# Kernel optimization log

Measured on AMD Instinct MI355X. Metric: run time of the kernel, lower is better.

## Reference

```python
import jax, jax.numpy as jnp
import numpy as np


def _pairwise_sqdist(x, y):
    # x: [B, N, D], y: [B, M, D] -> P: [B, N, M] squared euclidean distances
    xx = jnp.sum(x * x, axis=-1)              # [B, N]
    yy = jnp.sum(y * y, axis=-1)              # [B, M]
    zz = jnp.einsum('bnd,bmd->bnm', x, y)     # [B, N, M]
    return xx[:, :, None] + yy[:, None, :] - 2.0 * zz


def setup_inputs() -> dict:
    key = jax.random.key(0)
    k1, k2 = jax.random.split(key)
    B, N, D = 8, 8192, 3
    preds = jax.random.normal(k1, (B, N, D), dtype=jnp.float32)
    gts = jax.random.normal(k2, (B, N, D), dtype=jnp.float32)
    return {"preds": preds, "gts": gts}


def reference(preds, gts):
    # P = batch_pairwise_dist(gts, preds): P[b, i, j] = ||gts[b,i] - preds[b,j]||^2
    P = _pairwise_sqdist(gts, preds)          # [B, N_gts, N_preds]
    loss_1 = jnp.sum(jnp.min(P, axis=1))      # min over gts points
    loss_2 = jnp.sum(jnp.min(P, axis=2))      # min over pred points
    return loss_1 + loss_2
```

## Files before the change

### kernel.cpp

```cpp
#include <hip/hip_runtime.h>

typedef _Float16 f16;
typedef f16 half8 __attribute__((ext_vector_type(8)));
typedef float f32x16 __attribute__((ext_vector_type(16)));

#define BB 8
#define NN 8192
#define SETPTS (BB * NN)
#define NPTS (2 * SETPTS)
#define TQ NPTS

__device__ __forceinline__ void gload_lds16(const void* g, void* l) {
  __builtin_amdgcn_global_load_lds(
      (const __attribute__((address_space(1))) void*)g,
      (__attribute__((address_space(3))) void*)l, 16, 0, 0);
}

__global__ __launch_bounds__(256) void chamfer_prep(
    const float* __restrict__ preds, const float* __restrict__ gts,
    float* __restrict__ yy, half8* __restrict__ Aq, half8* __restrict__ Bq) {
  int idx = blockIdx.x * 256 + threadIdx.x;
  int s = idx >> 16;
  int off = idx & (SETPTS - 1);
  const float* src = s ? gts : preds;
  float x0 = src[off * 3 + 0], x1 = src[off * 3 + 1], x2 = src[off * 3 + 2];

  f16 h0 = (f16)x0; f16 l0 = (f16)(x0 - (float)h0);
  f16 h1 = (f16)x1; f16 l1 = (f16)(x1 - (float)h1);
  f16 h2 = (f16)x2; f16 l2 = (f16)(x2 - (float)h2);

  float Y0 = -2.f * x0, Y1 = -2.f * x1, Y2 = -2.f * x2;
  f16 H0 = (f16)Y0; f16 L0 = (f16)(Y0 - (float)H0);
  f16 H1 = (f16)Y1; f16 L1 = (f16)(Y1 - (float)H1);
  f16 H2 = (f16)Y2; f16 L2 = (f16)(Y2 - (float)H2);

  float yv = x0 * x0 + x1 * x1 + x2 * x2;
  f16 yh = (f16)yv; f16 yl = (f16)(yv - (float)yh);

  f16 one = (f16)1.f, zz = (f16)0.f;
  half8 A0 = {h0, l0, h0, l0, h1, l1, h1, l1};
  half8 A1 = {h2, l2, h2, l2, one, one, zz, zz};
  half8 B0 = {H0, H0, L0, L0, H1, H1, L1, L1};
  half8 B1 = {H2, H2, L2, L2, yh, yl, zz, zz};

  Aq[idx * 2 + 0] = A0; Aq[idx * 2 + 1] = A1;
  Bq[idx * 2 + 0] = B0; Bq[idx * 2 + 1] = B1;
  yy[idx] = yv;
}

template <int R>
__global__ __launch_bounds__(256, 4) void chamfer_mfma(
    const half8* __restrict__ Aq, const half8* __restrict__ Bq,
    float* __restrict__ partial) {
  constexpr int NSTEP = NN / R / 32;
  __shared__ __align__(16) char lds[NSTEP * 1024];

  int bi = blockIdx.x;
  int xcd = bi & 7;
  int idx = bi >> 3;
  int panel = xcd * 2 + (idx & 1);
  int dir = panel >> 3;
  int b = panel & 7;
  int sub = idx >> 1;
  int qb = sub & 31;
  int r = sub >> 5;

  int tid = threadIdx.x;
  int w = tid >> 6;
  int l = tid & 63;
  int l31 = l & 31;
  int lh = l >> 5;

  const half8* Qp =
      Aq + ((size_t)(dir * BB + b) * NN + qb * 256 + w * 64) * 2;
  half8 q0 = Qp[l31 * 2 + lh];
  half8 q1 = Qp[(32 + l31) * 2 + lh];

  const char* gpanel = (const char*)(Bq + ((size_t)((1 - dir) * BB + b) * NN +
                                           r * (NN / R)) * 2);
  int perm = ((l & 31) * 2 + (l >> 5)) * 16;

  {
    constexpr int TPW = NSTEP / 4;
    const char* csrc = gpanel + (size_t)(w * TPW) * 1024 + perm;
    char* cdst = &lds[w * TPW * 1024];
#pragma unroll
    for (int i = 0; i < TPW; ++i)
      gload_lds16(csrc + i * 1024, cdst + i * 1024);
  }

  f32x16 zero;
#pragma unroll
  for (int i = 0; i < 16; ++i) zero[i] = 0.f;
  float run0 = 3.4e38f, run1 = 3.4e38f;

  __syncthreads();

  const half8* lb = (const half8*)&lds[0];
#pragma unroll 4
  for (int st = 0; st < NSTEP; ++st) {
    half8 bt = lb[st * 64 + l];
    f32x16 oa = __builtin_amdgcn_mfma_f32_32x32x16_f16(bt, q0, zero, 0, 0, 0);
    f32x16 ob = __builtin_amdgcn_mfma_f32_32x32x16_f16(bt, q1, zero, 0, 0, 0);
    {
      float t0 = fminf(fminf(oa[0], oa[1]), oa[2]);
      float t1 = fminf(fminf(oa[3], oa[4]), oa[5]);
      float t2 = fminf(fminf(oa[6], oa[7]), oa[8]);
      float t3 = fminf(fminf(oa[9], oa[10]), oa[11]);
      float t4 = fminf(fminf(oa[12], oa[13]), oa[14]);
      float u0 = fminf(fminf(t0, t1), t2);
      float u1 = fminf(fminf(t3, t4), oa[15]);
      run0 = fminf(fminf(run0, u0), u1);
    }
    {
      float t0 = fminf(fminf(ob[0], ob[1]), ob[2]);
      float t1 = fminf(fminf(ob[3], ob[4]), ob[5]);
      float t2 = fminf(fminf(ob[6], ob[7]), ob[8]);
      float t3 = fminf(fminf(ob[9], ob[10]), ob[11]);
      float t4 = fminf(fminf(ob[12], ob[13]), ob[14]);
      float u0 = fminf(fminf(t0, t1), t2);
      float u1 = fminf(fminf(t3, t4), ob[15]);
      run1 = fminf(fminf(run1, u0), u1);
    }
  }

  float v0 = fminf(run0, __shfl_xor(run0, 32));
  float v1 = fminf(run1, __shfl_xor(run1, 32));

  size_t qflat = (size_t)(dir * BB + b) * NN + qb * 256 + w * 64;
  float* pr = partial + (size_t)r * TQ + qflat;
  if (lh == 0) {
    pr[l31] = v0;
    pr[32 + l31] = v1;
  }
}

template <int R>
__global__ __launch_bounds__(256) void chamfer_combine(
    const float* __restrict__ partial, const float* __restrict__ yy,
    float* __restrict__ bsums) {
  int q = blockIdx.x * 256 + threadIdx.x;
  float m = partial[q];
#pragma unroll
  for (int rr = 1; rr < R; ++rr) m = fminf(m, partial[(size_t)rr * TQ + q]);
  m += yy[q];
  __shared__ float s[256];
  s[threadIdx.x] = m;
  __syncthreads();
  for (int o = 128; o > 0; o >>= 1) {
    if (threadIdx.x < o) s[threadIdx.x] += s[threadIdx.x + o];
    __syncthreads();
  }
  if (threadIdx.x == 0) bsums[blockIdx.x] = s[0];
}

__global__ __launch_bounds__(256) void chamfer_final(
    const float* __restrict__ bsums, float* __restrict__ out, int n) {
  float v = 0.f;
  for (int i = threadIdx.x; i < n; i += 256) v += bsums[i];
  __shared__ float s[256];
  s[threadIdx.x] = v;
  __syncthreads();
  for (int o = 128; o > 0; o >>= 1) {
    if (threadIdx.x < o) s[threadIdx.x] += s[threadIdx.x + o];
    __syncthreads();
  }
  if (threadIdx.x == 0) out[0] = s[0];
}

extern "C" void kernel_launch(void* const* d_in, const int* in_sizes, int n_in,
                              void* d_out, int out_size, void* d_ws,
                              size_t ws_size, hipStream_t stream) {
  const float* preds = (const float*)d_in[0];
  const float* gts = (const float*)d_in[1];
  float* out = (float*)d_out;

  size_t fixed = (size_t)1024 * 4 + (size_t)NPTS * 4 + (size_t)NPTS * 64;
  int R = (ws_size >= (size_t)16 * TQ * 4 + fixed) ? 16 : 8;

  float* partial = (float*)d_ws;
  float* bsums = partial + (size_t)R * TQ;
  float* yy = bsums + 1024;
  half8* Aq = (half8*)(yy + NPTS);
  half8* Bq = Aq + (size_t)NPTS * 2;

  chamfer_prep<<<NPTS / 256, 256, 0, stream>>>(preds, gts, yy, Aq, Bq);
  if (R == 16) {
    chamfer_mfma<16><<<2 * BB * 32 * 16, 256, 0, stream>>>(Aq, Bq, partial);
    chamfer_combine<16><<<TQ / 256, 256, 0, stream>>>(partial, yy, bsums);
  } else {
    chamfer_mfma<8><<<2 * BB * 32 * 8, 256, 0, stream>>>(Aq, Bq, partial);
    chamfer_combine<8><<<TQ / 256, 256, 0, stream>>>(partial, yy, bsums);
  }
  chamfer_final<<<1, 256, 0, stream>>>(bsums, out, TQ / 256);
}
```

Before: 48.65 us.

## Stream reference tiles from global into registers instead of staging in LDS

The MFMA kernel no longer stages its reference panel into LDS with global_load_lds and a barrier. Each lane now loads its B fragment directly from global memory, with a two-step register prefetch across an unroll-by-two loop. The split factor R is fixed at 4, giving fewer blocks with longer loops and a smaller partial buffer for the combine pass. This removes LDS use and the block barrier, at the cost of relying on cache hits for the repeated global fragment loads and on fewer blocks to hide latency.

```diff
diff --git a/kernel.cpp b/kernel.cpp
--- a/kernel.cpp
+++ b/kernel.cpp
@@ -9,12 +9,6 @@
 #define SETPTS (BB * NN)
 #define NPTS (2 * SETPTS)
 #define TQ NPTS
-
-__device__ __forceinline__ void gload_lds16(const void* g, void* l) {
-  __builtin_amdgcn_global_load_lds(
-      (const __attribute__((address_space(1))) void*)g,
-      (__attribute__((address_space(3))) void*)l, 16, 0, 0);
-}
 
 __global__ __launch_bounds__(256) void chamfer_prep(
     const float* __restrict__ preds, const float* __restrict__ gts,
@@ -53,7 +47,6 @@
     const half8* __restrict__ Aq, const half8* __restrict__ Bq,
     float* __restrict__ partial) {
   constexpr int NSTEP = NN / R / 32;
-  __shared__ __align__(16) char lds[NSTEP * 1024];
 
   int bi = blockIdx.x;
   int xcd = bi & 7;
@@ -76,53 +69,49 @@
   half8 q0 = Qp[l31 * 2 + lh];
   half8 q1 = Qp[(32 + l31) * 2 + lh];
 
-  const char* gpanel = (const char*)(Bq + ((size_t)((1 - dir) * BB + b) * NN +
-                                           r * (NN / R)) * 2);
-  int perm = ((l & 31) * 2 + (l >> 5)) * 16;
-
-  {
-    constexpr int TPW = NSTEP / 4;
-    const char* csrc = gpanel + (size_t)(w * TPW) * 1024 + perm;
-    char* cdst = &lds[w * TPW * 1024];
-#pragma unroll
-    for (int i = 0; i < TPW; ++i)
-      gload_lds16(csrc + i * 1024, cdst + i * 1024);
-  }
+  const half8* Bl = Bq +
+                    ((size_t)((1 - dir) * BB + b) * NN + r * (NN / R)) * 2 +
+                    l31 * 2 + lh;
 
   f32x16 zero;
 #pragma unroll
   for (int i = 0; i < 16; ++i) zero[i] = 0.f;
   float run0 = 3.4e38f, run1 = 3.4e38f;
 
-  __syncthreads();
+#define MINTREE(o, run)                                   \
+  {                                                       \
+    float t0_ = fminf(fminf(o[0], o[1]), o[2]);           \
+    float t1_ = fminf(fminf(o[3], o[4]), o[5]);           \
+    float t2_ = fminf(fminf(o[6], o[7]), o[8]);           \
+    float t3_ = fminf(fminf(o[9], o[10]), o[11]);         \
+    float t4_ = fminf(fminf(o[12], o[13]), o[14]);        \
+    float u0_ = fminf(fminf(t0_, t1_), t2_);              \
+    float u1_ = fminf(fminf(t3_, t4_), o[15]);            \
+    run = fminf(fminf(run, u0_), u1_);                    \
+  }
 
-  const half8* lb = (const half8*)&lds[0];
-#pragma unroll 4
-  for (int st = 0; st < NSTEP; ++st) {
-    half8 bt = lb[st * 64 + l];
-    f32x16 oa = __builtin_amdgcn_mfma_f32_32x32x16_f16(bt, q0, zero, 0, 0, 0);
-    f32x16 ob = __builtin_amdgcn_mfma_f32_32x32x16_f16(bt, q1, zero, 0, 0, 0);
+  half8 t0 = Bl[0];
+  half8 t1 = Bl[64];
+#pragma unroll 1
+  for (int s = 0; s < NSTEP; s += 2) {
+    half8 t2 = Bl[(size_t)(((s + 2) & (NSTEP - 1)) * 64)];
     {
-      float t0 = fminf(fminf(oa[0], oa[1]), oa[2]);
-      float t1 = fminf(fminf(oa[3], oa[4]), oa[5]);
-      float t2 = fminf(fminf(oa[6], oa[7]), oa[8]);
-      float t3 = fminf(fminf(oa[9], oa[10]), oa[11]);
-      float t4 = fminf(fminf(oa[12], oa[13]), oa[14]);
-      float u0 = fminf(fminf(t0, t1), t2);
-      float u1 = fminf(fminf(t3, t4), oa[15]);
-      run0 = fminf(fminf(run0, u0), u1);
+      f32x16 oa = __builtin_amdgcn_mfma_f32_32x32x16_f16(t0, q0, zero, 0, 0, 0);
+      f32x16 ob = __builtin_amdgcn_mfma_f32_32x32x16_f16(t0, q1, zero, 0, 0, 0);
+      MINTREE(oa, run0)
+      MINTREE(ob, run1)
     }
+    half8 t3 = Bl[(size_t)(((s + 3) & (NSTEP - 1)) * 64)];
     {
-      float t0 = fminf(fminf(ob[0], ob[1]), ob[2]);
-      float t1 = fminf(fminf(ob[3], ob[4]), ob[5]);
-      float t2 = fminf(fminf(ob[6], ob[7]), ob[8]);
-      float t3 = fminf(fminf(ob[9], ob[10]), ob[11]);
-      float t4 = fminf(fminf(ob[12], ob[13]), ob[14]);
-      float u0 = fminf(fminf(t0, t1), t2);
-      float u1 = fminf(fminf(t3, t4), ob[15]);
-      run1 = fminf(fminf(run1, u0), u1);
+      f32x16 oc = __builtin_amdgcn_mfma_f32_32x32x16_f16(t1, q0, zero, 0, 0, 0);
+      f32x16 od = __builtin_amdgcn_mfma_f32_32x32x16_f16(t1, q1, zero, 0, 0, 0);
+      MINTREE(oc, run0)
+      MINTREE(od, run1)
     }
+    t0 = t2;
+    t1 = t3;
   }
+#undef MINTREE
 
   float v0 = fminf(run0, __shfl_xor(run0, 32));
   float v1 = fminf(run1, __shfl_xor(run1, 32));
@@ -175,9 +164,7 @@
   const float* gts = (const float*)d_in[1];
   float* out = (float*)d_out;
 
-  size_t fixed = (size_t)1024 * 4 + (size_t)NPTS * 4 + (size_t)NPTS * 64;
-  int R = (ws_size >= (size_t)16 * TQ * 4 + fixed) ? 16 : 8;
-
+  const int R = 4;
   float* partial = (float*)d_ws;
   float* bsums = partial + (size_t)R * TQ;
   float* yy = bsums + 1024;
@@ -185,12 +172,7 @@
   half8* Bq = Aq + (size_t)NPTS * 2;
 
   chamfer_prep<<<NPTS / 256, 256, 0, stream>>>(preds, gts, yy, Aq, Bq);
-  if (R == 16) {
-    chamfer_mfma<16><<<2 * BB * 32 * 16, 256, 0, stream>>>(Aq, Bq, partial);
-    chamfer_combine<16><<<TQ / 256, 256, 0, stream>>>(partial, yy, bsums);
-  } else {
-    chamfer_mfma<8><<<2 * BB * 32 * 8, 256, 0, stream>>>(Aq, Bq, partial);
-    chamfer_combine<8><<<TQ / 256, 256, 0, stream>>>(partial, yy, bsums);
-  }
+  chamfer_mfma<R><<<2 * BB * 32 * R, 256, 0, stream>>>(Aq, Bq, partial);
+  chamfer_combine<R><<<TQ / 256, 256, 0, stream>>>(partial, yy, bsums);
   chamfer_final<<<1, 256, 0, stream>>>(bsums, out, TQ / 256);
 }
```

New measurement: 48.32 us. Within noise of the previous version (-0.7%).
